# Kernel tuning notes

Measured on AMD Instinct MI355X. Metric: run time of the kernel, lower is better.

## Reference

```python
import jax, jax.numpy as jnp
import numpy as np

T, D, F, E, K = 8192, 1024, 512, 8, 2


def setup_inputs() -> dict:
    key = jax.random.key(0)
    k0, k1, k2, k3, k4 = jax.random.split(key, 5)
    hidden_states = jax.random.normal(k0, (T, D), dtype=jnp.float32)
    top_k_index = jax.random.randint(k1, (T, K), 0, E)
    top_k_weights = jax.random.uniform(k2, (T, K), dtype=jnp.float32)
    gate_up_proj = jax.random.normal(k3, (E, 2 * F, D), dtype=jnp.float32) * 0.02
    down_proj = jax.random.normal(k4, (E, D, F), dtype=jnp.float32) * 0.02
    return dict(hidden_states=hidden_states, top_k_index=top_k_index,
                top_k_weights=top_k_weights, gate_up_proj=gate_up_proj,
                down_proj=down_proj)


def reference(hidden_states, top_k_index, top_k_weights, gate_up_proj, down_proj):
    # hidden_states: [T, D]; top_k_index/weights: [T, K]
    # gate_up_proj: [E, 2F, D]; down_proj: [E, D, F]
    num_experts = gate_up_proj.shape[0]
    out = jnp.zeros_like(hidden_states)
    for e in range(num_experts):  # fixed small expert set
        # combined routing weight for expert e per token (sums duplicate k-slots,
        # matching index_add_ of per-slot contributions of identical expert output)
        w_e = jnp.sum(jnp.where(top_k_index == e, top_k_weights, 0.0), axis=-1)  # [T]
        gu = hidden_states @ gate_up_proj[e].T          # [T, 2F]
        gate, up = jnp.split(gu, 2, axis=-1)            # [T, F] each
        act = jax.nn.silu(gate) * up                    # SiLU-mul (LigerSiLUMulFunction)
        out = out + (act @ down_proj[e].T) * w_e[:, None]
    return out
```

## Files before the change

kernel.cpp:

```cpp
#include <hip/hip_runtime.h>
#include <cstdint>
#include <cstddef>

#define T_TOK 8192
#define DIM   1024
#define FF    512
#define NE    8
#define NSLOT 16384
#define BM    128
#define MAXBLK (NSLOT / BM + NE)

typedef short s16x8 __attribute__((ext_vector_type(8)));
typedef float f32x4 __attribute__((ext_vector_type(4)));

__device__ __forceinline__ unsigned int f2bf(float f) {
    union { float f; unsigned int u; } v; v.f = f;
    return (v.u + 0x7FFFu + ((v.u >> 16) & 1u)) >> 16;
}
__device__ __forceinline__ float bf2f(unsigned short b) {
    union { unsigned int u; float f; } v; v.u = ((unsigned int)b) << 16;
    return v.f;
}
__device__ __forceinline__ int pack2(float a, float b) {
    return (int)f2bf(a) | ((int)f2bf(b) << 16);
}
__device__ __forceinline__ int4 cvt8(const float* p) {
    float4 x = *(const float4*)p;
    float4 y = *(const float4*)(p + 4);
    int4 r;
    r.x = pack2(x.x, x.y); r.y = pack2(x.z, x.w);
    r.z = pack2(y.x, y.y); r.w = pack2(y.z, y.w);
    return r;
}

__device__ __forceinline__ void gload16(const unsigned short* g, unsigned short* l) {
    __builtin_amdgcn_global_load_lds(
        (const __attribute__((address_space(1))) void*)g,
        (__attribute__((address_space(3))) void*)l, 16, 0, 0);
}

__global__ __launch_bounds__(256) void route_count(const int* __restrict__ idx,
                                                   int* __restrict__ partial) {
    __shared__ int cnt[NE];
    const int tid = threadIdx.x;
    if (tid < NE) cnt[tid] = 0;
    __syncthreads();
    atomicAdd(&cnt[idx[blockIdx.x * 256 + tid]], 1);
    __syncthreads();
    if (tid < NE) partial[blockIdx.x * NE + tid] = cnt[tid];
}

__global__ void route_scan(const int* __restrict__ partial, int* offsets, int* cursor,
                           int* blk_e, int* blk_by) {
    __shared__ int counts_s[NE];
    const int tid = threadIdx.x;
    if (tid < NE) {
        int s = 0;
        for (int b = 0; b < 64; ++b) s += partial[b * NE + tid];
        counts_s[tid] = s;
    }
    __syncthreads();
    if (tid == 0) {
        int acc = 0, nb = 0;
        for (int e = 0; e < NE; ++e) {
            offsets[e] = acc; cursor[e] = acc;
            const int nby = (counts_s[e] + BM - 1) / BM;
            for (int b = 0; b < nby; ++b) { blk_e[nb] = e; blk_by[nb] = b; ++nb; }
            acc += counts_s[e];
        }
        offsets[NE] = acc;
        for (int b = nb; b < MAXBLK; ++b) { blk_e[b] = -1; blk_by[b] = 0; }
    }
}
__global__ void route_scatter(const int* __restrict__ idx, int* cursor,
                              int* row_slot, int* slot_pos) {
    int s = blockIdx.x * 256 + threadIdx.x;
    if (s < NSLOT) {
        int e = idx[s];
        int p = atomicAdd(&cursor[e], 1);
        row_slot[p] = s;
        slot_pos[s] = p;
    }
}

__global__ void cvt_all(const float* __restrict__ h, const float* __restrict__ g,
                        const float* __restrict__ d,
                        unsigned short* __restrict__ hb, unsigned short* __restrict__ gb,
                        unsigned short* __restrict__ db) {
    const int N1 = T_TOK * DIM / 8;
    const int N2 = NE * 2 * FF * DIM / 8;
    const int N3 = NE * DIM * FF / 8;
    const int stride = gridDim.x * 256;
    for (int i = blockIdx.x * 256 + threadIdx.x; i < N1 + N2 + N3; i += stride) {
        const float* s; unsigned short* o; int j;
        if (i < N1)            { s = h; o = hb; j = i; }
        else if (i < N1 + N2)  { s = g; o = gb; j = i - N1; }
        else                   { s = d; o = db; j = i - N1 - N2; }
        *(int4*)(o + (size_t)j * 8) = cvt8(s + (size_t)j * 8);
    }
}


__global__ __launch_bounds__(256) void gemm1_bf16(
    const unsigned short* __restrict__ hb,
    const unsigned short* __restrict__ gupb,
    const int* __restrict__ row_slot,
    const int* __restrict__ offsets,
    const int* __restrict__ blk_e,
    const int* __restrict__ blk_by,
    unsigned short* __restrict__ act)
{
    const int e = blk_e[blockIdx.y];
    if (e < 0) return;
    const int bx      = blockIdx.x;
    const int lby     = blk_by[blockIdx.y];
    const int rowbase = offsets[e] + lby * BM;
    const int rowlim  = offsets[e + 1] - 1;
    const int nrows   = min(BM, offsets[e + 1] - rowbase);

    __shared__ __align__(16) unsigned short Ab0[BM * 64], Ab1[BM * 64];
    __shared__ __align__(16) unsigned short Bb0[128 * 64], Bb1[128 * 64];

    const int tid  = threadIdx.x;
    const int lane = tid & 63;
    const int wv   = tid >> 6;
    const int wr   = wv >> 1, wc = wv & 1;

    int aoff[4];
#pragma unroll
    for (int i = 0; i < 4; ++i) {
        const int ch = tid + i * 256;
        const int r = ch >> 3, c = ch & 7;
        int grow = rowbase + r; if (grow > rowlim) grow = rowlim;
        const int tok = row_slot[grow] >> 1;
        aoff[i] = tok * DIM + ((c ^ (r & 7)) << 3);
    }
    int boff[4];
#pragma unroll
    for (int i = 0; i < 4; ++i) {
        const int ch = tid + i * 256;
        const int r = ch >> 3, c = ch & 7;
        const int gr = (r < 64) ? (bx * 64 + r) : (FF + bx * 64 + r - 64);
        boff[i] = e * (2 * FF * DIM) + gr * DIM + ((c ^ (r & 7)) << 3);
    }

    const f32x4 zf = {0.f, 0.f, 0.f, 0.f};
    f32x4 ag[4][2], au[4][2];
#pragma unroll
    for (int m = 0; m < 4; ++m)
#pragma unroll
        for (int n = 0; n < 2; ++n) { ag[m][n] = zf; au[m][n] = zf; }

    unsigned short *Ard = Ab0, *Awr = Ab1, *Brd = Bb0, *Bwr = Bb1;

#pragma unroll
    for (int i = 0; i < 4; ++i) gload16(hb + aoff[i],   Ard + (wv * 64 + i * 256) * 8);
#pragma unroll
    for (int i = 0; i < 4; ++i) gload16(gupb + boff[i], Brd + (wv * 64 + i * 256) * 8);
    __syncthreads();

#pragma unroll 1
    for (int t = 0; t < DIM / 64; ++t) {
        if (t < DIM / 64 - 1) {
            const int kn = (t + 1) * 64;
#pragma unroll
            for (int i = 0; i < 4; ++i) gload16(hb + aoff[i] + kn,   Awr + (wv * 64 + i * 256) * 8);
#pragma unroll
            for (int i = 0; i < 4; ++i) gload16(gupb + boff[i] + kn, Bwr + (wv * 64 + i * 256) * 8);
        }
        const char* Abc = (const char*)Ard;
        const char* Bbc = (const char*)Brd;
#pragma unroll
        for (int kk = 0; kk < 2; ++kk) {
            const int kc = kk * 4 + (lane >> 4);
            s16x8 af[4], bg[2], bu[2];
#pragma unroll
            for (int m = 0; m < 4; ++m) {
                const int r = wr * 64 + m * 16 + (lane & 15);
                af[m] = *(const s16x8*)(Abc + r * 128 + ((kc ^ (r & 7)) << 4));
            }
#pragma unroll
            for (int n = 0; n < 2; ++n) {
                const int rg = wc * 32 + n * 16 + (lane & 15);
                bg[n] = *(const s16x8*)(Bbc + rg * 128 + ((kc ^ (rg & 7)) << 4));
                const int ru = rg + 64;
                bu[n] = *(const s16x8*)(Bbc + ru * 128 + ((kc ^ (ru & 7)) << 4));
            }
#pragma unroll
            for (int m = 0; m < 4; ++m)
#pragma unroll
                for (int n = 0; n < 2; ++n) {
                    ag[m][n] = __builtin_amdgcn_mfma_f32_16x16x32_bf16(af[m], bg[n], ag[m][n], 0, 0, 0);
                    au[m][n] = __builtin_amdgcn_mfma_f32_16x16x32_bf16(af[m], bu[n], au[m][n], 0, 0, 0);
                }
        }
        __syncthreads();
        unsigned short* tp;
        tp = Ard; Ard = Awr; Awr = tp;
        tp = Brd; Brd = Bwr; Bwr = tp;
    }

#pragma unroll
    for (int m = 0; m < 4; ++m)
#pragma unroll
        for (int n = 0; n < 2; ++n) {
            const int col = bx * 64 + wc * 32 + n * 16 + (lane & 15);
#pragma unroll
            for (int i = 0; i < 4; ++i) {
                const int rl = wr * 64 + m * 16 + ((lane >> 4) << 2) + i;
                if (rl < nrows) {
                    const float g = ag[m][n][i];
                    const float u = au[m][n][i];
                    const float a = (g / (1.f + __expf(-g))) * u;
                    act[(size_t)(rowbase + rl) * FF + col] = (unsigned short)f2bf(a);
                }
            }
        }
}

template <int MODE>
__global__ __launch_bounds__(256) void gemm2_slot(
    const unsigned short* __restrict__ act,
    const unsigned short* __restrict__ downb,
    const int* __restrict__ row_slot,
    const int* __restrict__ offsets,
    const int* __restrict__ blk_e,
    const int* __restrict__ blk_by,
    void* __restrict__ outslot)
{
    const int e = blk_e[blockIdx.y];
    if (e < 0) return;
    const int bx      = blockIdx.x;
    const int lby     = blk_by[blockIdx.y];
    const int rowbase = offsets[e] + lby * BM;
    const int nrows   = min(BM, offsets[e + 1] - rowbase);
    const int rowlim  = offsets[e + 1] - 1;

    __shared__ __align__(16) unsigned short Ab0[BM * 64], Ab1[BM * 64];
    __shared__ __align__(16) unsigned short Bb0[128 * 64], Bb1[128 * 64];

    const int tid  = threadIdx.x;
    const int lane = tid & 63;
    const int wv   = tid >> 6;
    const int wr   = wv >> 1, wc = wv & 1;

    int aoff[4];
#pragma unroll
    for (int i = 0; i < 4; ++i) {
        const int ch = tid + i * 256;
        const int r = ch >> 3, c = ch & 7;
        int grow = rowbase + r; if (grow > rowlim) grow = rowlim;
        aoff[i] = grow * FF + ((c ^ (r & 7)) << 3);
    }
    int boff[4];
#pragma unroll
    for (int i = 0; i < 4; ++i) {
        const int ch = tid + i * 256;
        const int r = ch >> 3, c = ch & 7;
        boff[i] = e * (DIM * FF) + (bx * 128 + r) * FF + ((c ^ (r & 7)) << 3);
    }

    const f32x4 zf = {0.f, 0.f, 0.f, 0.f};
    f32x4 acc[4][4];
#pragma unroll
    for (int m = 0; m < 4; ++m)
#pragma unroll
        for (int n = 0; n < 4; ++n) acc[m][n] = zf;

    unsigned short *Ard = Ab0, *Awr = Ab1, *Brd = Bb0, *Bwr = Bb1;

#pragma unroll
    for (int i = 0; i < 4; ++i) gload16(act + aoff[i],   Ard + (wv * 64 + i * 256) * 8);
#pragma unroll
    for (int i = 0; i < 4; ++i) gload16(downb + boff[i], Brd + (wv * 64 + i * 256) * 8);
    __syncthreads();

#pragma unroll 1
    for (int t = 0; t < FF / 64; ++t) {
        if (t < FF / 64 - 1) {
            const int kn = (t + 1) * 64;
#pragma unroll
            for (int i = 0; i < 4; ++i) gload16(act + aoff[i] + kn,   Awr + (wv * 64 + i * 256) * 8);
#pragma unroll
            for (int i = 0; i < 4; ++i) gload16(downb + boff[i] + kn, Bwr + (wv * 64 + i * 256) * 8);
        }
        const char* Abc = (const char*)Ard;
        const char* Bbc = (const char*)Brd;
#pragma unroll
        for (int kk = 0; kk < 2; ++kk) {
            const int kc = kk * 4 + (lane >> 4);
            s16x8 af[4], bf[4];
#pragma unroll
            for (int m = 0; m < 4; ++m) {
                const int r = wr * 64 + m * 16 + (lane & 15);
                af[m] = *(const s16x8*)(Abc + r * 128 + ((kc ^ (r & 7)) << 4));
            }
#pragma unroll
            for (int n = 0; n < 4; ++n) {
                const int r = wc * 64 + n * 16 + (lane & 15);
                bf[n] = *(const s16x8*)(Bbc + r * 128 + ((kc ^ (r & 7)) << 4));
            }
#pragma unroll
            for (int m = 0; m < 4; ++m)
#pragma unroll
                for (int n = 0; n < 4; ++n)
                    acc[m][n] = __builtin_amdgcn_mfma_f32_16x16x32_bf16(af[m], bf[n], acc[m][n], 0, 0, 0);
        }
        __syncthreads();
        unsigned short* tp;
        tp = Ard; Ard = Awr; Awr = tp;
        tp = Brd; Brd = Bwr; Bwr = tp;
    }

#pragma unroll
    for (int m = 0; m < 4; ++m)
#pragma unroll
        for (int i = 0; i < 4; ++i) {
            const int rl = wr * 64 + m * 16 + ((lane >> 4) << 2) + i;
            if (rl < nrows) {
                const size_t base = (size_t)(rowbase + rl) * DIM + bx * 128 + wc * 64 + (lane & 15);
                if (MODE == 1) {
                    float* o = (float*)outslot + base;
#pragma unroll
                    for (int n = 0; n < 4; ++n) o[n * 16] = acc[m][n][i];
                } else {
                    unsigned short* o = (unsigned short*)outslot + base;
#pragma unroll
                    for (int n = 0; n < 4; ++n) o[n * 16] = (unsigned short)f2bf(acc[m][n][i]);
                }
            }
        }
}

template <int MODE>
__global__ __launch_bounds__(256) void combine_k(
    const void* __restrict__ outslot,
    const int* __restrict__ slot_pos,
    const float* __restrict__ tkw,
    float* __restrict__ out)
{
    const int i = blockIdx.x * 256 + threadIdx.x;
    const int t = i >> 7;
    const int d = (i & 127) << 3;
    const int p0 = slot_pos[2 * t], p1 = slot_pos[2 * t + 1];
    const float w0 = tkw[2 * t],    w1 = tkw[2 * t + 1];
    float r0[8], r1[8];
    if (MODE == 1) {
        const float* s0 = (const float*)outslot + (size_t)p0 * DIM + d;
        const float* s1 = (const float*)outslot + (size_t)p1 * DIM + d;
        float4 a0 = *(const float4*)s0, a1 = *(const float4*)(s0 + 4);
        float4 b0 = *(const float4*)s1, b1 = *(const float4*)(s1 + 4);
        r0[0]=a0.x; r0[1]=a0.y; r0[2]=a0.z; r0[3]=a0.w; r0[4]=a1.x; r0[5]=a1.y; r0[6]=a1.z; r0[7]=a1.w;
        r1[0]=b0.x; r1[1]=b0.y; r1[2]=b0.z; r1[3]=b0.w; r1[4]=b1.x; r1[5]=b1.y; r1[6]=b1.z; r1[7]=b1.w;
    } else {
        const s16x8 a = *(const s16x8*)((const unsigned short*)outslot + (size_t)p0 * DIM + d);
        const s16x8 b = *(const s16x8*)((const unsigned short*)outslot + (size_t)p1 * DIM + d);
#pragma unroll
        for (int j = 0; j < 8; ++j) { r0[j] = bf2f((unsigned short)a[j]); r1[j] = bf2f((unsigned short)b[j]); }
    }
    float4 o0, o1;
    o0.x = w0*r0[0]+w1*r1[0]; o0.y = w0*r0[1]+w1*r1[1]; o0.z = w0*r0[2]+w1*r1[2]; o0.w = w0*r0[3]+w1*r1[3];
    o1.x = w0*r0[4]+w1*r1[4]; o1.y = w0*r0[5]+w1*r1[5]; o1.z = w0*r0[6]+w1*r1[6]; o1.w = w0*r0[7]+w1*r1[7];
    float* op = out + (size_t)t * DIM + d;
    *(float4*)op = o0;
    *(float4*)(op + 4) = o1;
}


__global__ __launch_bounds__(256) void moe_gemm1(
    const float* __restrict__ hidden, const float* __restrict__ gup,
    const int* __restrict__ row_slot, const int* __restrict__ offsets,
    unsigned short* __restrict__ act)
{
    const int e = blockIdx.z;
    const int row0 = offsets[e];
    const int n_e = offsets[e + 1] - row0;
    const int by = blockIdx.y;
    if (by * 128 >= n_e) return;
    const int bx = blockIdx.x;
    __shared__ __align__(16) unsigned short Abuf[128 * 64];
    __shared__ __align__(16) unsigned short Bbuf[128 * 64];
    char* Ab = (char*)Abuf; char* Bb = (char*)Bbuf;
    const int tid = threadIdx.x, lane = tid & 63, wv = tid >> 6;
    const int wr = wv >> 1, wc = wv & 1;
    const float* aptr[4]; const float* bptr[4]; int soff[4];
#pragma unroll
    for (int i = 0; i < 4; ++i) {
        const int chunk = tid + i * 256;
        const int r = chunk >> 3, c = chunk & 7;
        soff[i] = r * 128 + ((c ^ (r & 7)) << 4);
        int rr = by * 128 + r; if (rr >= n_e) rr = n_e - 1;
        const int slot = row_slot[row0 + rr];
        aptr[i] = hidden + (size_t)(slot >> 1) * DIM + c * 8;
        const int gr = (r < 64) ? (bx * 64 + r) : (FF + bx * 64 + (r - 64));
        bptr[i] = gup + (size_t)e * (2 * FF * DIM) + (size_t)gr * DIM + c * 8;
    }
    const f32x4 zf = {0.f, 0.f, 0.f, 0.f};
    f32x4 acc_g[4][2], acc_u[4][2];
#pragma unroll
    for (int m = 0; m < 4; ++m)
#pragma unroll
        for (int n = 0; n < 2; ++n) { acc_g[m][n] = zf; acc_u[m][n] = zf; }
    for (int k0 = 0; k0 < DIM; k0 += 64) {
        __syncthreads();
#pragma unroll
        for (int i = 0; i < 4; ++i) *(int4*)(Ab + soff[i]) = cvt8(aptr[i] + k0);
#pragma unroll
        for (int i = 0; i < 4; ++i) *(int4*)(Bb + soff[i]) = cvt8(bptr[i] + k0);
        __syncthreads();
#pragma unroll
        for (int kk = 0; kk < 2; ++kk) {
            const int kc = kk * 4 + (lane >> 4);
            s16x8 af[4], bg[2], bu[2];
#pragma unroll
            for (int m = 0; m < 4; ++m) {
                const int r = wr * 64 + m * 16 + (lane & 15);
                af[m] = *(const s16x8*)(Ab + r * 128 + ((kc ^ (r & 7)) << 4));
            }
#pragma unroll
            for (int n = 0; n < 2; ++n) {
                const int rg = wc * 32 + n * 16 + (lane & 15);
                bg[n] = *(const s16x8*)(Bb + rg * 128 + ((kc ^ (rg & 7)) << 4));
                const int ru = rg + 64;
                bu[n] = *(const s16x8*)(Bb + ru * 128 + ((kc ^ (ru & 7)) << 4));
            }
#pragma unroll
            for (int m = 0; m < 4; ++m)
#pragma unroll
                for (int n = 0; n < 2; ++n) {
                    acc_g[m][n] = __builtin_amdgcn_mfma_f32_16x16x32_bf16(af[m], bg[n], acc_g[m][n], 0, 0, 0);
                    acc_u[m][n] = __builtin_amdgcn_mfma_f32_16x16x32_bf16(af[m], bu[n], acc_u[m][n], 0, 0, 0);
                }
        }
    }
#pragma unroll
    for (int m = 0; m < 4; ++m)
#pragma unroll
        for (int n = 0; n < 2; ++n) {
            const int col = bx * 64 + wc * 32 + n * 16 + (lane & 15);
#pragma unroll
            for (int i = 0; i < 4; ++i) {
                const int rl = wr * 64 + m * 16 + ((lane >> 4) << 2) + i;
                const int rr = by * 128 + rl;
                if (rr < n_e) {
                    const float g = acc_g[m][n][i];
                    const float u = acc_u[m][n][i];
                    const float a = (g / (1.f + __expf(-g))) * u;
                    act[(size_t)(row0 + rr) * FF + col] = (unsigned short)f2bf(a);
                }
            }
        }
}

__global__ __launch_bounds__(256) void moe_gemm2(
    const unsigned short* __restrict__ act, const float* __restrict__ down,
    const int* __restrict__ row_slot, const int* __restrict__ offsets,
    const float* __restrict__ tkw, float* __restrict__ out)
{
    const int e = blockIdx.z;
    const int row0 = offsets[e];
    const int n_e = offsets[e + 1] - row0;
    const int by = blockIdx.y;
    if (by * 128 >= n_e) return;
    const int bx = blockIdx.x;
    __shared__ __align__(16) unsigned short Abuf[128 * 64];
    __shared__ __align__(16) unsigned short Bbuf[128 * 64];
    char* Ab = (char*)Abuf; char* Bb = (char*)Bbuf;
    const int tid = threadIdx.x, lane = tid & 63, wv = tid >> 6;
    const int wr = wv >> 1, wc = wv & 1;
    const unsigned short* aptr[4]; const float* bptr[4]; int soff[4];
#pragma unroll
    for (int i = 0; i < 4; ++i) {
        const int chunk = tid + i * 256;
        const int r = chunk >> 3, c = chunk & 7;
        soff[i] = r * 128 + ((c ^ (r & 7)) << 4);
        int rr = by * 128 + r; if (rr >= n_e) rr = n_e - 1;
        aptr[i] = act + (size_t)(row0 + rr) * FF + c * 8;
        bptr[i] = down + (size_t)e * (DIM * FF) + (size_t)(bx * 128 + r) * FF + c * 8;
    }
    const f32x4 zf = {0.f, 0.f, 0.f, 0.f};
    f32x4 acc[4][4];
#pragma unroll
    for (int m = 0; m < 4; ++m)
#pragma unroll
        for (int n = 0; n < 4; ++n) acc[m][n] = zf;
    for (int k0 = 0; k0 < FF; k0 += 64) {
        __syncthreads();
#pragma unroll
        for (int i = 0; i < 4; ++i) *(int4*)(Ab + soff[i]) = *(const int4*)(aptr[i] + k0);
#pragma unroll
        for (int i = 0; i < 4; ++i) *(int4*)(Bb + soff[i]) = cvt8(bptr[i] + k0);
        __syncthreads();
#pragma unroll
        for (int kk = 0; kk < 2; ++kk) {
            const int kc = kk * 4 + (lane >> 4);
            s16x8 af[4], bf[4];
#pragma unroll
            for (int m = 0; m < 4; ++m) {
                const int r = wr * 64 + m * 16 + (lane & 15);
                af[m] = *(const s16x8*)(Ab + r * 128 + ((kc ^ (r & 7)) << 4));
            }
#pragma unroll
            for (int n = 0; n < 4; ++n) {
                const int r = wc * 64 + n * 16 + (lane & 15);
                bf[n] = *(const s16x8*)(Bb + r * 128 + ((kc ^ (r & 7)) << 4));
            }
#pragma unroll
            for (int m = 0; m < 4; ++m)
#pragma unroll
                for (int n = 0; n < 4; ++n)
                    acc[m][n] = __builtin_amdgcn_mfma_f32_16x16x32_bf16(af[m], bf[n], acc[m][n], 0, 0, 0);
        }
    }
#pragma unroll
    for (int m = 0; m < 4; ++m)
#pragma unroll
        for (int i = 0; i < 4; ++i) {
            const int rl = wr * 64 + m * 16 + ((lane >> 4) << 2) + i;
            const int rr = by * 128 + rl;
            if (rr < n_e) {
                const int slot = row_slot[row0 + rr];
                const float w = tkw[slot];
                float* orow = out + (size_t)(slot >> 1) * DIM + bx * 128 + wc * 64 + (lane & 15);
#pragma unroll
                for (int n = 0; n < 4; ++n)
                    unsafeAtomicAdd(orow + n * 16, acc[m][n][i] * w);
            }
        }
}

extern "C" void kernel_launch(void* const* d_in, const int* in_sizes, int n_in,
                              void* d_out, int out_size, void* d_ws, size_t ws_size,
                              hipStream_t stream)
{
    const float* hidden = (const float*)d_in[0];
    const int*   idx    = (const int*)  d_in[1];
    const float* tkw    = (const float*)d_in[2];
    const float* gup    = (const float*)d_in[3];
    const float* down   = (const float*)d_in[4];
    float* out = (float*)d_out;

    const size_t ACT = (size_t)NSLOT * FF * 2;
    const size_t HB  = (size_t)T_TOK * DIM * 2;
    const size_t GB  = (size_t)NE * 2 * FF * DIM * 2;
    const size_t DB  = (size_t)NE * DIM * FF * 2;
    const size_t RS  = (size_t)NSLOT * 4;
    const size_t SP  = (size_t)NSLOT * 4;
    const size_t CTRL = 8192;
    const size_t OS32 = (size_t)NSLOT * DIM * 4;
    const size_t OS16 = (size_t)NSLOT * DIM * 2;
    char* ws = (char*)d_ws;
    unsigned short* act = (unsigned short*)ws;

    const size_t base_need = ACT + HB + GB + DB + RS + SP + CTRL;
    int mode;
    if      (ws_size >= base_need + OS32) mode = 1;
    else if (ws_size >= base_need + OS16) mode = 2;
    else if (ws_size >= ACT + RS + SP + CTRL) mode = 0;
    else mode = -1;
    if (mode < 0) return;

    unsigned short *hb = nullptr, *gb = nullptr, *db = nullptr;
    int *row_slot, *ctrl; void* outslot = nullptr;
    if (mode == 1 || mode == 2) {
        hb = (unsigned short*)(ws + ACT);
        gb = (unsigned short*)(ws + ACT + HB);
        db = (unsigned short*)(ws + ACT + HB + GB);
        row_slot = (int*)(ws + ACT + HB + GB + DB);
        ctrl     = (int*)(ws + ACT + HB + GB + DB + RS + SP);
        outslot  = (void*)(ws + base_need);
    } else {
        row_slot = (int*)(ws + ACT);
        ctrl     = (int*)(ws + ACT + RS + SP);
    }
    int* slot_pos = row_slot + NSLOT;
    int* offsets = ctrl;
    int* blk_e   = ctrl + 16;
    int* blk_by  = ctrl + 16 + MAXBLK;
    int* cursor  = ctrl + 16 + 2 * MAXBLK;
    int* partial = cursor + 8;

    if (mode == 0)
        hipMemsetAsync(out, 0, (size_t)T_TOK * DIM * sizeof(float), stream);

    route_count  <<<NSLOT / 256, 256, 0, stream>>>(idx, partial);
    route_scan   <<<1, 64, 0, stream>>>(partial, offsets, cursor, blk_e, blk_by);
    route_scatter<<<NSLOT / 256, 256, 0, stream>>>(idx, cursor, row_slot, slot_pos);

    if (mode == 1 || mode == 2) {
        cvt_all<<<2048, 256, 0, stream>>>(hidden, gup, down, hb, gb, db);
        gemm1_bf16<<<dim3(FF / 64, MAXBLK), 256, 0, stream>>>(
            hb, gb, row_slot, offsets, blk_e, blk_by, act);
        if (mode == 1) {
            gemm2_slot<1><<<dim3(DIM / 128, MAXBLK), 256, 0, stream>>>(
                act, db, row_slot, offsets, blk_e, blk_by, outslot);
            combine_k<1><<<T_TOK * DIM / 8 / 256, 256, 0, stream>>>(outslot, slot_pos, tkw, out);
        } else {
            gemm2_slot<2><<<dim3(DIM / 128, MAXBLK), 256, 0, stream>>>(
                act, db, row_slot, offsets, blk_e, blk_by, outslot);
            combine_k<2><<<T_TOK * DIM / 8 / 256, 256, 0, stream>>>(outslot, slot_pos, tkw, out);
        }
    } else {
        moe_gemm1<<<dim3(FF / 64, 128, NE), 256, 0, stream>>>(hidden, gup, row_slot, offsets, act);
        moe_gemm2<<<dim3(DIM / 128, 128, NE), 256, 0, stream>>>(act, down, row_slot, offsets, tkw, out);
    }
}
```

Measured before the change: 206.3 us.

## Scatter weighted bf16 expert outputs by slot and simplify combine

The down-projection GEMM now multiplies each row by its routing weight and writes bf16 results straight into the original slot position, not the sorted position. The combine kernel then reads contiguous pairs of slot rows and just adds them, so slot_pos and its scatter writes are no longer needed. The fp32 intermediate path is removed, which halves intermediate traffic when workspace is large. In exchange, the GEMM epilogue writes rows scattered by slot, and weighted outputs are rounded to bf16 before summation, which may cost some precision.

```diff
diff --git a/kernel.cpp b/kernel.cpp
--- a/kernel.cpp
+++ b/kernel.cpp
@@ -73,13 +73,12 @@
     }
 }
 __global__ void route_scatter(const int* __restrict__ idx, int* cursor,
-                              int* row_slot, int* slot_pos) {
+                              int* row_slot) {
     int s = blockIdx.x * 256 + threadIdx.x;
     if (s < NSLOT) {
         int e = idx[s];
         int p = atomicAdd(&cursor[e], 1);
         row_slot[p] = s;
-        slot_pos[s] = p;
     }
 }
 
@@ -218,7 +217,6 @@
         }
 }
 
-template <int MODE>
 __global__ __launch_bounds__(256) void gemm2_slot(
     const unsigned short* __restrict__ act,
     const unsigned short* __restrict__ downb,
@@ -226,7 +224,8 @@
     const int* __restrict__ offsets,
     const int* __restrict__ blk_e,
     const int* __restrict__ blk_by,
-    void* __restrict__ outslot)
+    const float* __restrict__ tkw,
+    unsigned short* __restrict__ outslot)
 {
     const int e = blk_e[blockIdx.y];
     if (e < 0) return;
@@ -318,49 +317,34 @@
         for (int i = 0; i < 4; ++i) {
             const int rl = wr * 64 + m * 16 + ((lane >> 4) << 2) + i;
             if (rl < nrows) {
-                const size_t base = (size_t)(rowbase + rl) * DIM + bx * 128 + wc * 64 + (lane & 15);
-                if (MODE == 1) {
-                    float* o = (float*)outslot + base;
-#pragma unroll
-                    for (int n = 0; n < 4; ++n) o[n * 16] = acc[m][n][i];
-                } else {
-                    unsigned short* o = (unsigned short*)outslot + base;
-#pragma unroll
-                    for (int n = 0; n < 4; ++n) o[n * 16] = (unsigned short)f2bf(acc[m][n][i]);
-                }
-            }
-        }
-}
-
-template <int MODE>
+                const int slot = row_slot[rowbase + rl];
+                const float w  = tkw[slot];
+                unsigned short* o = outslot + (size_t)slot * DIM + bx * 128 + wc * 64 + (lane & 15);
+#pragma unroll
+                for (int n = 0; n < 4; ++n)
+                    o[n * 16] = (unsigned short)f2bf(acc[m][n][i] * w);
+            }
+        }
+}
+
 __global__ __launch_bounds__(256) void combine_k(
-    const void* __restrict__ outslot,
-    const int* __restrict__ slot_pos,
-    const float* __restrict__ tkw,
+    const unsigned short* __restrict__ outslot,
     float* __restrict__ out)
 {
     const int i = blockIdx.x * 256 + threadIdx.x;
     const int t = i >> 7;
     const int d = (i & 127) << 3;
-    const int p0 = slot_pos[2 * t], p1 = slot_pos[2 * t + 1];
-    const float w0 = tkw[2 * t],    w1 = tkw[2 * t + 1];
-    float r0[8], r1[8];
-    if (MODE == 1) {
-        const float* s0 = (const float*)outslot + (size_t)p0 * DIM + d;
-        const float* s1 = (const float*)outslot + (size_t)p1 * DIM + d;
-        float4 a0 = *(const float4*)s0, a1 = *(const float4*)(s0 + 4);
-        float4 b0 = *(const float4*)s1, b1 = *(const float4*)(s1 + 4);
-        r0[0]=a0.x; r0[1]=a0.y; r0[2]=a0.z; r0[3]=a0.w; r0[4]=a1.x; r0[5]=a1.y; r0[6]=a1.z; r0[7]=a1.w;
-        r1[0]=b0.x; r1[1]=b0.y; r1[2]=b0.z; r1[3]=b0.w; r1[4]=b1.x; r1[5]=b1.y; r1[6]=b1.z; r1[7]=b1.w;
-    } else {
-        const s16x8 a = *(const s16x8*)((const unsigned short*)outslot + (size_t)p0 * DIM + d);
-        const s16x8 b = *(const s16x8*)((const unsigned short*)outslot + (size_t)p1 * DIM + d);
-#pragma unroll
-        for (int j = 0; j < 8; ++j) { r0[j] = bf2f((unsigned short)a[j]); r1[j] = bf2f((unsigned short)b[j]); }
-    }
+    const s16x8 a = *(const s16x8*)(outslot + (size_t)(2 * t) * DIM + d);
+    const s16x8 b = *(const s16x8*)(outslot + (size_t)(2 * t + 1) * DIM + d);
     float4 o0, o1;
-    o0.x = w0*r0[0]+w1*r1[0]; o0.y = w0*r0[1]+w1*r1[1]; o0.z = w0*r0[2]+w1*r1[2]; o0.w = w0*r0[3]+w1*r1[3];
-    o1.x = w0*r0[4]+w1*r1[4]; o1.y = w0*r0[5]+w1*r1[5]; o1.z = w0*r0[6]+w1*r1[6]; o1.w = w0*r0[7]+w1*r1[7];
+    o0.x = bf2f((unsigned short)a[0]) + bf2f((unsigned short)b[0]);
+    o0.y = bf2f((unsigned short)a[1]) + bf2f((unsigned short)b[1]);
+    o0.z = bf2f((unsigned short)a[2]) + bf2f((unsigned short)b[2]);
+    o0.w = bf2f((unsigned short)a[3]) + bf2f((unsigned short)b[3]);
+    o1.x = bf2f((unsigned short)a[4]) + bf2f((unsigned short)b[4]);
+    o1.y = bf2f((unsigned short)a[5]) + bf2f((unsigned short)b[5]);
+    o1.z = bf2f((unsigned short)a[6]) + bf2f((unsigned short)b[6]);
+    o1.w = bf2f((unsigned short)a[7]) + bf2f((unsigned short)b[7]);
     float* op = out + (size_t)t * DIM + d;
     *(float4*)op = o0;
     *(float4*)(op + 4) = o1;
@@ -545,35 +529,31 @@
     const size_t GB  = (size_t)NE * 2 * FF * DIM * 2;
     const size_t DB  = (size_t)NE * DIM * FF * 2;
     const size_t RS  = (size_t)NSLOT * 4;
-    const size_t SP  = (size_t)NSLOT * 4;
     const size_t CTRL = 8192;
-    const size_t OS32 = (size_t)NSLOT * DIM * 4;
-    const size_t OS16 = (size_t)NSLOT * DIM * 2;
+    const size_t OSB = (size_t)NSLOT * DIM * 2;
     char* ws = (char*)d_ws;
     unsigned short* act = (unsigned short*)ws;
 
-    const size_t base_need = ACT + HB + GB + DB + RS + SP + CTRL;
+    const size_t base_need = ACT + HB + GB + DB + RS + CTRL;
     int mode;
-    if      (ws_size >= base_need + OS32) mode = 1;
-    else if (ws_size >= base_need + OS16) mode = 2;
-    else if (ws_size >= ACT + RS + SP + CTRL) mode = 0;
+    if      (ws_size >= base_need + OSB) mode = 1;
+    else if (ws_size >= ACT + RS + CTRL) mode = 0;
     else mode = -1;
     if (mode < 0) return;
 
     unsigned short *hb = nullptr, *gb = nullptr, *db = nullptr;
-    int *row_slot, *ctrl; void* outslot = nullptr;
-    if (mode == 1 || mode == 2) {
+    int *row_slot, *ctrl; unsigned short* outslot = nullptr;
+    if (mode == 1) {
         hb = (unsigned short*)(ws + ACT);
         gb = (unsigned short*)(ws + ACT + HB);
         db = (unsigned short*)(ws + ACT + HB + GB);
         row_slot = (int*)(ws + ACT + HB + GB + DB);
-        ctrl     = (int*)(ws + ACT + HB + GB + DB + RS + SP);
-        outslot  = (void*)(ws + base_need);
+        ctrl     = (int*)(ws + ACT + HB + GB + DB + RS);
+        outslot  = (unsigned short*)(ws + base_need);
     } else {
         row_slot = (int*)(ws + ACT);
-        ctrl     = (int*)(ws + ACT + RS + SP);
-    }
-    int* slot_pos = row_slot + NSLOT;
+        ctrl     = (int*)(ws + ACT + RS);
+    }
     int* offsets = ctrl;
     int* blk_e   = ctrl + 16;
     int* blk_by  = ctrl + 16 + MAXBLK;
@@ -585,21 +565,15 @@
 
     route_count  <<<NSLOT / 256, 256, 0, stream>>>(idx, partial);
     route_scan   <<<1, 64, 0, stream>>>(partial, offsets, cursor, blk_e, blk_by);
-    route_scatter<<<NSLOT / 256, 256, 0, stream>>>(idx, cursor, row_slot, slot_pos);
-
-    if (mode == 1 || mode == 2) {
+    route_scatter<<<NSLOT / 256, 256, 0, stream>>>(idx, cursor, row_slot);
+
+    if (mode == 1) {
         cvt_all<<<2048, 256, 0, stream>>>(hidden, gup, down, hb, gb, db);
         gemm1_bf16<<<dim3(FF / 64, MAXBLK), 256, 0, stream>>>(
             hb, gb, row_slot, offsets, blk_e, blk_by, act);
-        if (mode == 1) {
-            gemm2_slot<1><<<dim3(DIM / 128, MAXBLK), 256, 0, stream>>>(
-                act, db, row_slot, offsets, blk_e, blk_by, outslot);
-            combine_k<1><<<T_TOK * DIM / 8 / 256, 256, 0, stream>>>(outslot, slot_pos, tkw, out);
-        } else {
-            gemm2_slot<2><<<dim3(DIM / 128, MAXBLK), 256, 0, stream>>>(
-                act, db, row_slot, offsets, blk_e, blk_by, outslot);
-            combine_k<2><<<T_TOK * DIM / 8 / 256, 256, 0, stream>>>(outslot, slot_pos, tkw, out);
-        }
+        gemm2_slot<<<dim3(DIM / 128, MAXBLK), 256, 0, stream>>>(
+            act, db, row_slot, offsets, blk_e, blk_by, tkw, outslot);
+        combine_k<<<T_TOK * DIM / 8 / 256, 256, 0, stream>>>(outslot, out);
     } else {
         moe_gemm1<<<dim3(FF / 64, 128, NE), 256, 0, stream>>>(hidden, gup, row_slot, offsets, act);
         moe_gemm2<<<dim3(DIM / 128, 128, NE), 256, 0, stream>>>(act, down, row_slot, offsets, tkw, out);
```

New measurement: 211.5 us. 2.5% more time.
